# Kernel optimization log

Hardware: AMD Instinct MI355X
Metric: run time of the kernel (lower is better)

## Reference

```python
import jax, jax.numpy as jnp
import numpy as np


def _conv1x1(x, w):
    # x [N,I,D,H,W], w [O,I]
    return jnp.einsum('nidhw,oi->nodhw', x, w)


def _conv3x3(x, w):
    return jax.lax.conv_general_dilated(
        x, w, window_strides=(1, 1, 1), padding=[(1, 1)] * 3,
        dimension_numbers=('NCDHW', 'OIDHW', 'NCDHW'))


def _interp_axis(x, out_len, axis):
    # linear interpolation along one axis, align_corners=True
    in_len = x.shape[axis]
    scale = (in_len - 1) / (out_len - 1)
    pos = jnp.arange(out_len, dtype=x.dtype) * scale
    lo = jnp.clip(jnp.floor(pos).astype(jnp.int32), 0, in_len - 1)
    hi = jnp.minimum(lo + 1, in_len - 1)
    frac = pos - lo.astype(x.dtype)
    shp = [1] * x.ndim
    shp[axis] = out_len
    frac = frac.reshape(shp)
    return jnp.take(x, lo, axis=axis) * (1 - frac) + jnp.take(x, hi, axis=axis) * frac


def _upsample_trilinear_ac(x, size):
    for ax, s in zip((2, 3, 4), size):
        x = _interp_axis(x, s, ax)
    return x


def _grid_sample_3d(inp, grid):
    # inp [N,C,D,H,W]; grid [N,Do,Ho,Wo,3] with channels (x=w, y=h, z=d) in [-1,1]
    # matches torch grid_sample defaults: trilinear, align_corners=False, zeros padding
    N, C, D, H, W = inp.shape
    ix = ((grid[..., 0] + 1) * W - 1) * 0.5
    iy = ((grid[..., 1] + 1) * H - 1) * 0.5
    iz = ((grid[..., 2] + 1) * D - 1) * 0.5
    x0 = jnp.floor(ix).astype(jnp.int32)
    y0 = jnp.floor(iy).astype(jnp.int32)
    z0 = jnp.floor(iz).astype(jnp.int32)
    fx = ix - x0.astype(inp.dtype)
    fy = iy - y0.astype(inp.dtype)
    fz = iz - z0.astype(inp.dtype)
    flat = inp.reshape(N, C, D * H * W)
    out = jnp.zeros((N, C) + grid.shape[1:4], dtype=inp.dtype)
    for dz, wz in ((0, 1 - fz), (1, fz)):
        for dy, wy in ((0, 1 - fy), (1, fy)):
            for dx, wx in ((0, 1 - fx), (1, fx)):
                zc = z0 + dz
                yc = y0 + dy
                xc = x0 + dx
                valid = (zc >= 0) & (zc < D) & (yc >= 0) & (yc < H) & (xc >= 0) & (xc < W)
                idx = (jnp.clip(zc, 0, D - 1) * H + jnp.clip(yc, 0, H - 1)) * W + jnp.clip(xc, 0, W - 1)
                vals = jax.vmap(lambda f, i: f[:, i])(flat, idx)  # [N,C,Do,Ho,Wo]
                w = (wz * wy * wx) * valid.astype(inp.dtype)
                out = out + vals * w[:, None]
    return out


def _point_reinforce(x, w_atten, w_conv):
    # SE-style: global avg pool -> 1x1 conv -> sigmoid -> residual scale -> 1x1 conv
    pooled = jnp.mean(x, axis=(2, 3, 4), keepdims=True)
    atten = jax.nn.sigmoid(_conv1x1(pooled, w_atten))
    x = x + x * atten
    return _conv1x1(x, w_conv)


def _forward(x, y, w_down_h, w_down_l, w_flow, w_att_atten, w_att_conv):
    D, H, W = x.shape[2:]
    low = _conv1x1(x, w_down_l)
    low = _point_reinforce(low, w_att_atten, w_att_conv)
    hf = _conv1x1(y, w_down_h)
    hf = _upsample_trilinear_ac(hf, (D, H, W))
    flow = _conv3x3(jnp.concatenate([hf, low], axis=1), w_flow)  # [N,3,D,H,W]
    # coordinate grid, channel order (w, h, d) as in the original flow_warp
    gw = jnp.broadcast_to(jnp.arange(W, dtype=x.dtype)[None, None, :], (D, H, W))
    gh = jnp.broadcast_to(jnp.arange(H, dtype=x.dtype)[None, :, None], (D, H, W))
    gd = jnp.broadcast_to(jnp.arange(D, dtype=x.dtype)[:, None, None], (D, H, W))
    grid = jnp.stack([gw, gh, gd], axis=0)[None]  # [1,3,D,H,W]
    norm = jnp.array([W, H, D], dtype=x.dtype)
    # NOTE: faithful to original -- divides by size only (grid ends up in [0,1), not [-1,1])
    vgrid = jnp.transpose(grid + flow, (0, 2, 3, 4, 1)) / norm  # [N,D,H,W,3]
    return _grid_sample_3d(y, vgrid)


def setup_inputs() -> dict:
    key = jax.random.key(0)
    ks = jax.random.split(key, 7)
    inplane_l, inplane_h, outplane = 64, 128, 64
    x = jax.random.normal(ks[0], (2, inplane_l, 16, 64, 64), dtype=jnp.float32)
    y = jax.random.normal(ks[1], (2, inplane_h, 8, 32, 32), dtype=jnp.float32)
    s = 0.05
    w_down_h = jax.random.normal(ks[2], (outplane, inplane_h), dtype=jnp.float32) * s
    w_down_l = jax.random.normal(ks[3], (outplane, inplane_l), dtype=jnp.float32) * s
    w_flow = jax.random.normal(ks[4], (3, 2 * outplane, 3, 3, 3), dtype=jnp.float32) * s
    w_att_atten = jax.random.normal(ks[5], (inplane_l, inplane_l), dtype=jnp.float32) * s
    w_att_conv = jax.random.normal(ks[6], (inplane_l, inplane_l), dtype=jnp.float32) * s
    return {'x': x, 'y': y, 'w_down_h': w_down_h, 'w_down_l': w_down_l,
            'w_flow': w_flow, 'w_att_atten': w_att_atten, 'w_att_conv': w_att_conv}


def reference(x, y, w_down_h, w_down_l, w_flow, w_att_atten, w_att_conv):
    return _forward(x, y, w_down_h, w_down_l, w_flow, w_att_atten, w_att_conv)
```

## Files before the change

### kernel.cpp

```cpp
#include <hip/hip_runtime.h>
#include <math.h>


#define MEANX_OFF  0
#define WCOMBT_OFF 128
#define HF_OFF     8320
#define LOW2_OFF   1056896
#define HFUP_OFF   9445504
#define VG_OFF     17834112
#define ZPAGE_OFF  18227328

__global__ void kmean(const float* __restrict__ x, float* __restrict__ meanx,
                      float* __restrict__ zpage) {
    if (blockIdx.x == 0 && threadIdx.x < 64) zpage[threadIdx.x] = 0.f;
    int ch = blockIdx.x;
    const float4* base = (const float4*)(x + (size_t)ch * 65536);
    float s = 0.f;
    for (int j = threadIdx.x; j < 16384; j += 256) {
        float4 v = base[j];
        s += v.x + v.y + v.z + v.w;
    }
    __shared__ float red[256];
    red[threadIdx.x] = s;
    __syncthreads();
    for (int off = 128; off > 0; off >>= 1) {
        if (threadIdx.x < off) red[threadIdx.x] += red[threadIdx.x + off];
        __syncthreads();
    }
    if (threadIdx.x == 0) meanx[ch] = red[0] * (1.0f / 65536.0f);
}

__global__ __launch_bounds__(256) void kprep(const float* __restrict__ wdl,
                                             const float* __restrict__ watt,
                                             const float* __restrict__ wconv,
                                             const float* __restrict__ meanx,
                                             float* __restrict__ wcombT) {
    const int n = blockIdx.x;
    const int tid = threadIdx.x;
    __shared__ float s_wdl[4096];
    __shared__ float s_wcT[4096];
    __shared__ float pooled[64], sc[64];
    for (int k = tid; k < 4096; k += 256) {
        s_wdl[k] = wdl[k];
        int o = k >> 6, j = k & 63;
        s_wcT[j * 64 + o] = wconv[k];
    }
    __syncthreads();
    if (tid < 64) {
        float p = 0.f;
        for (int i = 0; i < 64; ++i) p += s_wdl[tid * 64 + i] * meanx[n * 64 + i];
        pooled[tid] = p;
    }
    __syncthreads();
    if (tid < 64) {
        float a = 0.f;
        for (int i = 0; i < 64; ++i) a += watt[tid * 64 + i] * pooled[i];
        sc[tid] = 1.f + 1.f / (1.f + expf(-a));
    }
    __syncthreads();
    for (int k = 0; k < 16; ++k) {
        const int idx = tid + 256 * k;
        const int o = idx & 63, i = idx >> 6;
        float acc = 0.f;
#pragma unroll 8
        for (int j = 0; j < 64; ++j)
            acc += s_wcT[j * 64 + o] * (sc[j] * s_wdl[j * 64 + i]);
        wcombT[n * 4096 + i * 64 + o] = acc;
    }
}

__global__ __launch_bounds__(256) void kconv1l(const float* __restrict__ x,
                                               const float* __restrict__ wcombT,
                                               float* __restrict__ low2) {
    const int b = blockIdx.x;
    const int n = b >> 9;
    const int r = b & 511;
    const int os = r & 1;
    const int tile = r >> 1;
    const int p = tile * 256 + threadIdx.x;
    const float* xb = x + (size_t)n * 64 * 65536 + p;
    const float* wr = wcombT + n * 4096 + os * 32;

    float acc[32];
#pragma unroll
    for (int o = 0; o < 32; ++o) acc[o] = 0.f;

    for (int i = 0; i < 64; i += 2) {
        const float xi0 = xb[(size_t)(i + 0) * 65536];
        const float xi1 = xb[(size_t)(i + 1) * 65536];
#pragma unroll
        for (int o = 0; o < 32; ++o) {
            acc[o] = fmaf(wr[(i + 0) * 64 + o], xi0, acc[o]);
            acc[o] = fmaf(wr[(i + 1) * 64 + o], xi1, acc[o]);
        }
    }
    float* ob = low2 + (size_t)(n * 64 + os * 32) * 65536 + p;
#pragma unroll
    for (int o = 0; o < 32; ++o)
        ob[(size_t)o * 65536] = acc[o];
}

__global__ __launch_bounds__(256) void kconvh(const float* __restrict__ y,
                                              const float* __restrict__ wdh,
                                              float* __restrict__ hf) {
    const int b = blockIdx.x;
    const int n = b >> 7;
    const int r = b & 127;
    const int os = r & 3;
    const int tile = r >> 2;
    const int p = tile * 256 + threadIdx.x;
    const float* yb = y + (size_t)n * 128 * 8192 + p;

    float acc[16];
#pragma unroll
    for (int o = 0; o < 16; ++o) acc[o] = 0.f;

    for (int i = 0; i < 128; i += 2) {
        const float yi0 = yb[(size_t)(i + 0) * 8192];
        const float yi1 = yb[(size_t)(i + 1) * 8192];
#pragma unroll
        for (int o = 0; o < 16; ++o) {
            acc[o] = fmaf(wdh[(os * 16 + o) * 128 + i + 0], yi0, acc[o]);
            acc[o] = fmaf(wdh[(os * 16 + o) * 128 + i + 1], yi1, acc[o]);
        }
    }
    float* ob = hf + (size_t)(n * 64 + os * 16) * 8192 + p;
#pragma unroll
    for (int o = 0; o < 16; ++o)
        ob[(size_t)o * 8192] = acc[o];
}

__global__ __launch_bounds__(256) void kups(const float* __restrict__ hf,
                                            float* __restrict__ hfup) {
    int id2 = blockIdx.x * 256 + threadIdx.x;
    int wp = id2 & 31, h = (id2 >> 5) & 63, d = (id2 >> 11) & 15;
    int c = (id2 >> 15) & 63, n = id2 >> 21;
    const float SD = 7.0f / 15.0f, SH = 31.0f / 63.0f;
    float pd = (float)d * SD, ph = (float)h * SH;
    int z0 = (int)pd; if (z0 > 7) z0 = 7;
    int z1 = min(z0 + 1, 7); float fz = pd - (float)z0;
    int y0 = (int)ph; if (y0 > 31) y0 = 31;
    int y1 = min(y0 + 1, 31); float fy = ph - (float)y0;

    const int w0i = 2 * wp, w1i = 2 * wp + 1;
    float pw0 = (float)w0i * SH, pw1 = (float)w1i * SH;
    int xa = (int)pw0; if (xa > 31) xa = 31;
    float fx0 = pw0 - (float)xa;
    int xb = (int)pw1; if (xb > 31) xb = 31;
    float fx1 = pw1 - (float)xb;

    const float* b = hf + (size_t)(n * 64 + c) * 8192;
    const int r00 = (z0 * 32 + y0) * 32, r01 = (z0 * 32 + y1) * 32;
    const int r10 = (z1 * 32 + y0) * 32, r11 = (z1 * 32 + y1) * 32;
    const float wzy00 = (1.f - fz) * (1.f - fy), wzy01 = (1.f - fz) * fy;
    const float wzy10 = fz * (1.f - fy), wzy11 = fz * fy;

    float colv[3];
#pragma unroll
    for (int j = 0; j < 3; ++j) {
        int xc = min(xa + j, 31);
        colv[j] = wzy00 * b[r00 + xc] + wzy01 * b[r01 + xc] +
                  wzy10 * b[r10 + xc] + wzy11 * b[r11 + xc];
    }
    float o0 = colv[0] + (colv[1] - colv[0]) * fx0;
    int i1 = xb - xa;
    float lo = (i1 == 0) ? colv[0] : colv[1];
    float hi = (i1 == 0) ? colv[1] : colv[2];
    float o1 = lo + (hi - lo) * fx1;

    *(float2*)(hfup + ((size_t)id2 * 2)) = make_float2(o0, o1);
}

__global__ __launch_bounds__(256) void kflowp(const float* __restrict__ ws,
                                              const float* __restrict__ wflow,
                                              float* __restrict__ part) {
    const int tid = threadIdx.x;
    const int b = blockIdx.x;
    const int split = b & 15;
    const int tile = b >> 4;
    const int n = tile >> 6;
    const int t = tile & 63;
    const int td = t >> 4, th = (t >> 2) & 3, tw = t & 3;
    const int d0 = td * 4, h0 = th * 16, w0 = tw * 16;
    const int xo = tid & 3, ty = (tid >> 2) & 15, tz = tid >> 6;
    const int wv = tid >> 6;

    __shared__ float lds[3][2048];

    const int srcb = (split < 8)
        ? HFUP_OFF + (n * 64 + split * 8) * 65536
        : LOW2_OFF + (n * 64 + (split - 8) * 8) * 65536;

    int woff[8];
#pragma unroll
    for (int k = 0; k < 8; ++k) {
        const int e = tid + 256 * k;
        const int r = e / 18;
        const int lx = e - r * 18;
        const int z = r / 18;
        const int ly = r - z * 18;
        const int gz = d0 - 1 + z, gy = h0 - 1 + ly, gx = w0 - 1 + lx;
        const bool ok = (e < 1944) && ((unsigned)gz < 16u) && ((unsigned)gy < 64u) &&
                        ((unsigned)gx < 64u);
        woff[k] = ok ? (srcb + gz * 4096 + gy * 64 + gx) : ZPAGE_OFF;
    }

#define STAGE(BUFI, CI)                                                               \
    {                                                                                 \
        _Pragma("unroll")                                                             \
        for (int k = 0; k < 8; ++k) {                                                 \
            const int off = woff[k] + ((woff[k] < ZPAGE_OFF) ? (CI) * 65536 : 0);     \
            __builtin_amdgcn_global_load_lds(                                         \
                (const __attribute__((address_space(1))) unsigned int*)(ws + off),    \
                (__attribute__((address_space(3))) unsigned int*)                     \
                    (&lds[BUFI][wv * 64 + 256 * k]),                                  \
                4, 0, 0);                                                             \
        }                                                                             \
    }

    float acc[3][4];
#pragma unroll
    for (int o = 0; o < 3; ++o)
#pragma unroll
        for (int j = 0; j < 4; ++j) acc[o][j] = 0.f;

    STAGE(0, 0);

    for (int ci = 0; ci < 8; ++ci) {
        const int cur = ci % 3;
        if (ci < 7) {
            STAGE((ci + 1) % 3, ci + 1);
            asm volatile("s_waitcnt vmcnt(8)" ::: "memory");
        } else {
            asm volatile("s_waitcnt vmcnt(0)" ::: "memory");
        }
        __builtin_amdgcn_s_barrier();
        __builtin_amdgcn_sched_barrier(0);

        const int cgs = __builtin_amdgcn_readfirstlane(split * 8 + ci);
        const float* wb = wflow + (size_t)cgs * 27;
        const float* buf = lds[cur];
#pragma unroll
        for (int dz = 0; dz < 3; ++dz) {
#pragma unroll
            for (int dy = 0; dy < 3; ++dy) {
                const float* rp = &buf[((tz + dz) * 18 + ty + dy) * 18 + 4 * xo];
                const float2 a0 = *(const float2*)(rp);
                const float2 a1 = *(const float2*)(rp + 2);
                const float2 a2 = *(const float2*)(rp + 4);
                const float v[6] = {a0.x, a0.y, a1.x, a1.y, a2.x, a2.y};
                float wq[3][3];
#pragma unroll
                for (int o = 0; o < 3; ++o)
#pragma unroll
                    for (int dx = 0; dx < 3; ++dx)
                        wq[o][dx] = wb[o * 3456 + (dz * 3 + dy) * 3 + dx];
#pragma unroll
                for (int o = 0; o < 3; ++o)
#pragma unroll
                    for (int j = 0; j < 4; ++j)
#pragma unroll
                        for (int dx = 0; dx < 3; ++dx)
                            acc[o][j] = fmaf(wq[o][dx], v[j + dx], acc[o][j]);
            }
        }
    }
#undef STAGE

    const int oz = d0 + tz, oy = h0 + ty, ox = w0 + 4 * xo;
    const size_t base = ((size_t)(split * 2 + n)) * 3 * 65536;
    const int p = oz * 4096 + oy * 64 + ox;
#pragma unroll
    for (int o = 0; o < 3; ++o)
        *(float4*)(part + base + (size_t)o * 65536 + p) =
            make_float4(acc[o][0], acc[o][1], acc[o][2], acc[o][3]);
}

__global__ void kcomb(const float* __restrict__ part, float* __restrict__ vg) {
    int gid = blockIdx.x * 256 + threadIdx.x;
    int n = gid >> 16, p = gid & 65535;
    float s0 = 0.f, s1 = 0.f, s2 = 0.f;
    for (int s = 0; s < 16; ++s) {
        const float* bp = part + ((size_t)(s * 2 + n)) * 3 * 65536 + p;
        s0 += bp[0];
        s1 += bp[65536];
        s2 += bp[131072];
    }
    int w = p & 63, h = (p >> 6) & 63, d = p >> 12;
    size_t vb = (size_t)n * 3 * 65536;
    vg[vb + p]          = ((float)w + s0) * (1.0f / 64.0f);
    vg[vb + 65536 + p]  = ((float)h + s1) * (1.0f / 64.0f);
    vg[vb + 131072 + p] = ((float)d + s2) * (1.0f / 16.0f);
}

__global__ __launch_bounds__(256) void ktrans(const float* __restrict__ y,
                                              float* __restrict__ yt) {
    int b = blockIdx.x;
    int n = b >> 8;
    int rem = b & 255;
    int ct = rem >> 7, st = rem & 127;
    int c0 = ct * 64, s0 = st * 64;
    __shared__ float t[64][65];
    int tx = threadIdx.x & 63, ty = threadIdx.x >> 6;
#pragma unroll
    for (int k = 0; k < 16; ++k)
        t[ty + 4 * k][tx] = y[((size_t)(n * 128 + c0 + ty + 4 * k)) * 8192 + s0 + tx];
    __syncthreads();
#pragma unroll
    for (int k = 0; k < 16; ++k)
        yt[((size_t)(n * 8192 + s0 + ty + 4 * k)) * 128 + c0 + tx] = t[tx][ty + 4 * k];
}

__global__ __launch_bounds__(256) void ksample(const float* __restrict__ yt,
                                               const float* __restrict__ vg,
                                               float* __restrict__ out) {
    const int b = blockIdx.x;
    const int n = b >> 10;
    const int p0 = (b & 1023) << 6;
    const int tid = threadIdx.x;
    const int lane = tid & 63;
    const int wv = tid >> 6;

    __shared__ float lds[128 * 65];

    const float* ytn = yt + (size_t)n * 8192 * 128;
    const size_t vb = (size_t)n * 3 * 65536;

    for (int q = 0; q < 16; ++q) {
        const int pt = wv * 16 + q;
        const int p = p0 + pt;
        float gx = vg[vb + p], gy = vg[vb + 65536 + p], gz = vg[vb + 131072 + p];
        float ix = ((gx + 1.f) * 32.f - 1.f) * 0.5f;
        float iy = ((gy + 1.f) * 32.f - 1.f) * 0.5f;
        float iz = ((gz + 1.f) * 8.f - 1.f) * 0.5f;
        int x0 = (int)floorf(ix), y0 = (int)floorf(iy), z0 = (int)floorf(iz);
        float fx = ix - (float)x0, fy = iy - (float)y0, fz = iz - (float)z0;
        float wx[2] = {1.f - fx, fx}, wy[2] = {1.f - fy, fy}, wz[2] = {1.f - fz, fz};
        int idx8[8];
        float w8[8];
        float wsum = 0.f;
#pragma unroll
        for (int k = 0; k < 8; ++k) {
            int dz = k >> 2, dy = (k >> 1) & 1, dx = k & 1;
            int zc = z0 + dz, yc = y0 + dy, xc = x0 + dx;
            bool valid = ((unsigned)zc < 8u) && ((unsigned)yc < 32u) && ((unsigned)xc < 32u);
            int zcl = min(max(zc, 0), 7), ycl = min(max(yc, 0), 31), xcl = min(max(xc, 0), 31);
            idx8[k] = (zcl * 32 + ycl) * 32 + xcl;
            float wgt = wz[dz] * wy[dy] * wx[dx];
            w8[k] = valid ? wgt : 0.f;
            wsum += w8[k];
        }
        float ax = 0.f, ay = 0.f;
        if (wsum != 0.f) {
#pragma unroll
            for (int k = 0; k < 8; ++k) {
                const float2 v = *(const float2*)(ytn + (size_t)idx8[k] * 128 + 2 * lane);
                ax = fmaf(w8[k], v.x, ax);
                ay = fmaf(w8[k], v.y, ay);
            }
        }
        lds[(2 * lane) * 65 + pt] = ax;
        lds[(2 * lane + 1) * 65 + pt] = ay;
    }
    __syncthreads();
    const int pw = tid & 63, cw = tid >> 6;
    float* ob = out + (size_t)n * 128 * 65536 + p0 + pw;
#pragma unroll
    for (int k = 0; k < 32; ++k) {
        int c = k * 4 + cw;
        ob[(size_t)c * 65536] = lds[c * 65 + pw];
    }
}

extern "C" void kernel_launch(void* const* d_in, const int* in_sizes, int n_in,
                              void* d_out, int out_size, void* d_ws, size_t ws_size,
                              hipStream_t stream) {
    const float* x     = (const float*)d_in[0];
    const float* y     = (const float*)d_in[1];
    const float* wdh   = (const float*)d_in[2];
    const float* wdl   = (const float*)d_in[3];
    const float* wflow = (const float*)d_in[4];
    const float* watt  = (const float*)d_in[5];
    const float* wconv = (const float*)d_in[6];
    float* out = (float*)d_out;

    float* ws     = (float*)d_ws;
    float* meanx  = ws + MEANX_OFF;
    float* wcombT = ws + WCOMBT_OFF;
    float* hf     = ws + HF_OFF;
    float* low2   = ws + LOW2_OFF;
    float* hfup   = ws + HFUP_OFF;
    float* vg     = ws + VG_OFF;
    float* zpage  = ws + ZPAGE_OFF;

    float* part = out;
    float* yt = hfup;

    kmean<<<128, 256, 0, stream>>>(x, meanx, zpage);
    kprep<<<2, 256, 0, stream>>>(wdl, watt, wconv, meanx, wcombT);
    kconv1l<<<1024, 256, 0, stream>>>(x, wcombT, low2);
    kconvh<<<256, 256, 0, stream>>>(y, wdh, hf);
    kups<<<16384, 256, 0, stream>>>(hf, hfup);
    kflowp<<<2048, 256, 0, stream>>>(ws, wflow, part);
    kcomb<<<512, 256, 0, stream>>>(part, vg);
    ktrans<<<512, 256, 0, stream>>>(y, yt);
    ksample<<<2048, 256, 0, stream>>>(yt, vg, out);
}
```

Baseline: 195.8 us.

## Register-block two output depth slices per thread in flow conv, unroll 1x1 conv loops

```diff
diff --git a/kernel.cpp b/kernel.cpp
--- a/kernel.cpp
+++ b/kernel.cpp
@@ -85,13 +85,19 @@
 #pragma unroll
     for (int o = 0; o < 32; ++o) acc[o] = 0.f;
 
-    for (int i = 0; i < 64; i += 2) {
+    for (int i = 0; i < 64; i += 4) {
         const float xi0 = xb[(size_t)(i + 0) * 65536];
         const float xi1 = xb[(size_t)(i + 1) * 65536];
+        const float xi2 = xb[(size_t)(i + 2) * 65536];
+        const float xi3 = xb[(size_t)(i + 3) * 65536];
 #pragma unroll
         for (int o = 0; o < 32; ++o) {
-            acc[o] = fmaf(wr[(i + 0) * 64 + o], xi0, acc[o]);
-            acc[o] = fmaf(wr[(i + 1) * 64 + o], xi1, acc[o]);
+            float a = acc[o];
+            a = fmaf(wr[(i + 0) * 64 + o], xi0, a);
+            a = fmaf(wr[(i + 1) * 64 + o], xi1, a);
+            a = fmaf(wr[(i + 2) * 64 + o], xi2, a);
+            a = fmaf(wr[(i + 3) * 64 + o], xi3, a);
+            acc[o] = a;
         }
     }
     float* ob = low2 + (size_t)(n * 64 + os * 32) * 65536 + p;
@@ -115,13 +121,19 @@
 #pragma unroll
     for (int o = 0; o < 16; ++o) acc[o] = 0.f;
 
-    for (int i = 0; i < 128; i += 2) {
+    for (int i = 0; i < 128; i += 4) {
         const float yi0 = yb[(size_t)(i + 0) * 8192];
         const float yi1 = yb[(size_t)(i + 1) * 8192];
+        const float yi2 = yb[(size_t)(i + 2) * 8192];
+        const float yi3 = yb[(size_t)(i + 3) * 8192];
 #pragma unroll
         for (int o = 0; o < 16; ++o) {
-            acc[o] = fmaf(wdh[(os * 16 + o) * 128 + i + 0], yi0, acc[o]);
-            acc[o] = fmaf(wdh[(os * 16 + o) * 128 + i + 1], yi1, acc[o]);
+            float a = acc[o];
+            a = fmaf(wdh[(os * 16 + o) * 128 + i + 0], yi0, a);
+            a = fmaf(wdh[(os * 16 + o) * 128 + i + 1], yi1, a);
+            a = fmaf(wdh[(os * 16 + o) * 128 + i + 2], yi2, a);
+            a = fmaf(wdh[(os * 16 + o) * 128 + i + 3], yi3, a);
+            acc[o] = a;
         }
     }
     float* ob = hf + (size_t)(n * 64 + os * 16) * 8192 + p;
@@ -171,7 +183,7 @@
     *(float2*)(hfup + ((size_t)id2 * 2)) = make_float2(o0, o1);
 }
 
-__global__ __launch_bounds__(256) void kflowp(const float* __restrict__ ws,
+__global__ __launch_bounds__(128) void kflowp(const float* __restrict__ ws,
                                               const float* __restrict__ wflow,
                                               float* __restrict__ part) {
     const int tid = threadIdx.x;
@@ -182,7 +194,7 @@
     const int t = tile & 63;
     const int td = t >> 4, th = (t >> 2) & 3, tw = t & 3;
     const int d0 = td * 4, h0 = th * 16, w0 = tw * 16;
-    const int xo = tid & 3, ty = (tid >> 2) & 15, tz = tid >> 6;
+    const int xo = tid & 3, ty = (tid >> 2) & 15, tzp = tid >> 6;
     const int wv = tid >> 6;
 
     __shared__ float lds[3][2048];
@@ -191,10 +203,10 @@
         ? HFUP_OFF + (n * 64 + split * 8) * 65536
         : LOW2_OFF + (n * 64 + (split - 8) * 8) * 65536;
 
-    int woff[8];
-#pragma unroll
-    for (int k = 0; k < 8; ++k) {
-        const int e = tid + 256 * k;
+    int woff[16];
+#pragma unroll
+    for (int k = 0; k < 16; ++k) {
+        const int e = tid + 128 * k;
         const int r = e / 18;
         const int lx = e - r * 18;
         const int z = r / 18;
@@ -208,21 +220,23 @@
 #define STAGE(BUFI, CI)                                                               \
     {                                                                                 \
         _Pragma("unroll")                                                             \
-        for (int k = 0; k < 8; ++k) {                                                 \
+        for (int k = 0; k < 16; ++k) {                                                \
             const int off = woff[k] + ((woff[k] < ZPAGE_OFF) ? (CI) * 65536 : 0);     \
             __builtin_amdgcn_global_load_lds(                                         \
                 (const __attribute__((address_space(1))) unsigned int*)(ws + off),    \
                 (__attribute__((address_space(3))) unsigned int*)                     \
-                    (&lds[BUFI][wv * 64 + 256 * k]),                                  \
+                    (&lds[BUFI][wv * 64 + 128 * k]),                                  \
                 4, 0, 0);                                                             \
         }                                                                             \
     }
 
-    float acc[3][4];
+    float acc[3][2][4];
 #pragma unroll
     for (int o = 0; o < 3; ++o)
 #pragma unroll
-        for (int j = 0; j < 4; ++j) acc[o][j] = 0.f;
+        for (int q = 0; q < 2; ++q)
+#pragma unroll
+            for (int j = 0; j < 4; ++j) acc[o][q][j] = 0.f;
 
     STAGE(0, 0);
 
@@ -230,7 +244,7 @@
         const int cur = ci % 3;
         if (ci < 7) {
             STAGE((ci + 1) % 3, ci + 1);
-            asm volatile("s_waitcnt vmcnt(8)" ::: "memory");
+            asm volatile("s_waitcnt vmcnt(16)" ::: "memory");
         } else {
             asm volatile("s_waitcnt vmcnt(0)" ::: "memory");
         }
@@ -241,39 +255,49 @@
         const float* wb = wflow + (size_t)cgs * 27;
         const float* buf = lds[cur];
 #pragma unroll
-        for (int dz = 0; dz < 3; ++dz) {
+        for (int pi = 0; pi < 4; ++pi) {
+            const int pz = 2 * tzp + pi;
 #pragma unroll
             for (int dy = 0; dy < 3; ++dy) {
-                const float* rp = &buf[((tz + dz) * 18 + ty + dy) * 18 + 4 * xo];
+                const float* rp = &buf[(pz * 18 + ty + dy) * 18 + 4 * xo];
                 const float2 a0 = *(const float2*)(rp);
                 const float2 a1 = *(const float2*)(rp + 2);
                 const float2 a2 = *(const float2*)(rp + 4);
                 const float v[6] = {a0.x, a0.y, a1.x, a1.y, a2.x, a2.y};
-                float wq[3][3];
-#pragma unroll
-                for (int o = 0; o < 3; ++o)
-#pragma unroll
-                    for (int dx = 0; dx < 3; ++dx)
-                        wq[o][dx] = wb[o * 3456 + (dz * 3 + dy) * 3 + dx];
-#pragma unroll
-                for (int o = 0; o < 3; ++o)
-#pragma unroll
-                    for (int j = 0; j < 4; ++j)
-#pragma unroll
-                        for (int dx = 0; dx < 3; ++dx)
-                            acc[o][j] = fmaf(wq[o][dx], v[j + dx], acc[o][j]);
+#pragma unroll
+                for (int q = 0; q < 2; ++q) {
+                    const int dz = pi - q;
+                    if (dz < 0 || dz > 2) continue;
+#pragma unroll
+                    for (int o = 0; o < 3; ++o) {
+                        const float w0q = wb[o * 3456 + (dz * 3 + dy) * 3 + 0];
+                        const float w1q = wb[o * 3456 + (dz * 3 + dy) * 3 + 1];
+                        const float w2q = wb[o * 3456 + (dz * 3 + dy) * 3 + 2];
+#pragma unroll
+                        for (int j = 0; j < 4; ++j) {
+                            float a = acc[o][q][j];
+                            a = fmaf(w0q, v[j + 0], a);
+                            a = fmaf(w1q, v[j + 1], a);
+                            a = fmaf(w2q, v[j + 2], a);
+                            acc[o][q][j] = a;
+                        }
+                    }
+                }
             }
         }
     }
 #undef STAGE
 
-    const int oz = d0 + tz, oy = h0 + ty, ox = w0 + 4 * xo;
+    const int oy = h0 + ty, ox = w0 + 4 * xo;
     const size_t base = ((size_t)(split * 2 + n)) * 3 * 65536;
-    const int p = oz * 4096 + oy * 64 + ox;
 #pragma unroll
     for (int o = 0; o < 3; ++o)
-        *(float4*)(part + base + (size_t)o * 65536 + p) =
-            make_float4(acc[o][0], acc[o][1], acc[o][2], acc[o][3]);
+#pragma unroll
+        for (int q = 0; q < 2; ++q) {
+            const int oz = d0 + 2 * tzp + q;
+            *(float4*)(part + base + (size_t)o * 65536 + oz * 4096 + oy * 64 + ox) =
+                make_float4(acc[o][q][0], acc[o][q][1], acc[o][q][2], acc[o][q][3]);
+        }
 }
 
 __global__ void kcomb(const float* __restrict__ part, float* __restrict__ vg) {
@@ -401,7 +425,7 @@
     kconv1l<<<1024, 256, 0, stream>>>(x, wcombT, low2);
     kconvh<<<256, 256, 0, stream>>>(y, wdh, hf);
     kups<<<16384, 256, 0, stream>>>(hf, hfup);
-    kflowp<<<2048, 256, 0, stream>>>(ws, wflow, part);
+    kflowp<<<2048, 128, 0, stream>>>(ws, wflow, part);
     kcomb<<<512, 256, 0, stream>>>(part, vg);
     ktrans<<<512, 256, 0, stream>>>(y, yt);
     ksample<<<2048, 256, 0, stream>>>(yt, vg, out);
```

After: 208.5 us. +6.5%, slower.

## Merge independent kernels into combined launches via block-range dispatch

Applied to the files above, without the earlier changes.

```diff
diff --git a/kernel.cpp b/kernel.cpp
--- a/kernel.cpp
+++ b/kernel.cpp
@@ -10,24 +10,63 @@
 #define VG_OFF     17834112
 #define ZPAGE_OFF  18227328
 
-__global__ void kmean(const float* __restrict__ x, float* __restrict__ meanx,
-                      float* __restrict__ zpage) {
-    if (blockIdx.x == 0 && threadIdx.x < 64) zpage[threadIdx.x] = 0.f;
-    int ch = blockIdx.x;
-    const float4* base = (const float4*)(x + (size_t)ch * 65536);
-    float s = 0.f;
-    for (int j = threadIdx.x; j < 16384; j += 256) {
-        float4 v = base[j];
-        s += v.x + v.y + v.z + v.w;
-    }
-    __shared__ float red[256];
-    red[threadIdx.x] = s;
-    __syncthreads();
-    for (int off = 128; off > 0; off >>= 1) {
-        if (threadIdx.x < off) red[threadIdx.x] += red[threadIdx.x + off];
+__global__ __launch_bounds__(256) void kearly(const float* __restrict__ x,
+                                              const float* __restrict__ y,
+                                              const float* __restrict__ wdh,
+                                              float* __restrict__ meanx,
+                                              float* __restrict__ hf,
+                                              float* __restrict__ zpage) {
+    const int blk = blockIdx.x;
+    if (blk < 128) {
+        if (blk == 0 && threadIdx.x < 64) zpage[threadIdx.x] = 0.f;
+        int ch = blk;
+        const float4* base = (const float4*)(x + (size_t)ch * 65536);
+        float s = 0.f;
+        for (int j = threadIdx.x; j < 16384; j += 256) {
+            float4 v = base[j];
+            s += v.x + v.y + v.z + v.w;
+        }
+        __shared__ float red[256];
+        red[threadIdx.x] = s;
         __syncthreads();
-    }
-    if (threadIdx.x == 0) meanx[ch] = red[0] * (1.0f / 65536.0f);
+        for (int off = 128; off > 0; off >>= 1) {
+            if (threadIdx.x < off) red[threadIdx.x] += red[threadIdx.x + off];
+            __syncthreads();
+        }
+        if (threadIdx.x == 0) meanx[ch] = red[0] * (1.0f / 65536.0f);
+    } else {
+        const int b = blk - 128;
+        const int n = b >> 7;
+        const int r = b & 127;
+        const int os = r & 3;
+        const int tile = r >> 2;
+        const int p = tile * 256 + threadIdx.x;
+        const float* yb = y + (size_t)n * 128 * 8192 + p;
+
+        float acc[16];
+#pragma unroll
+        for (int o = 0; o < 16; ++o) acc[o] = 0.f;
+
+        for (int i = 0; i < 128; i += 4) {
+            const float yi0 = yb[(size_t)(i + 0) * 8192];
+            const float yi1 = yb[(size_t)(i + 1) * 8192];
+            const float yi2 = yb[(size_t)(i + 2) * 8192];
+            const float yi3 = yb[(size_t)(i + 3) * 8192];
+#pragma unroll
+            for (int o = 0; o < 16; ++o) {
+                float a = acc[o];
+                a = fmaf(wdh[(os * 16 + o) * 128 + i + 0], yi0, a);
+                a = fmaf(wdh[(os * 16 + o) * 128 + i + 1], yi1, a);
+                a = fmaf(wdh[(os * 16 + o) * 128 + i + 2], yi2, a);
+                a = fmaf(wdh[(os * 16 + o) * 128 + i + 3], yi3, a);
+                acc[o] = a;
+            }
+        }
+        float* ob = hf + (size_t)(n * 64 + os * 16) * 8192 + p;
+#pragma unroll
+        for (int o = 0; o < 16; ++o)
+            ob[(size_t)o * 8192] = acc[o];
+    }
 }
 
 __global__ __launch_bounds__(256) void kprep(const float* __restrict__ wdl,
@@ -69,106 +108,84 @@
     }
 }
 
-__global__ __launch_bounds__(256) void kconv1l(const float* __restrict__ x,
-                                               const float* __restrict__ wcombT,
-                                               float* __restrict__ low2) {
-    const int b = blockIdx.x;
-    const int n = b >> 9;
-    const int r = b & 511;
-    const int os = r & 1;
-    const int tile = r >> 1;
-    const int p = tile * 256 + threadIdx.x;
-    const float* xb = x + (size_t)n * 64 * 65536 + p;
-    const float* wr = wcombT + n * 4096 + os * 32;
-
-    float acc[32];
-#pragma unroll
-    for (int o = 0; o < 32; ++o) acc[o] = 0.f;
-
-    for (int i = 0; i < 64; i += 2) {
-        const float xi0 = xb[(size_t)(i + 0) * 65536];
-        const float xi1 = xb[(size_t)(i + 1) * 65536];
-#pragma unroll
-        for (int o = 0; o < 32; ++o) {
-            acc[o] = fmaf(wr[(i + 0) * 64 + o], xi0, acc[o]);
-            acc[o] = fmaf(wr[(i + 1) * 64 + o], xi1, acc[o]);
-        }
-    }
-    float* ob = low2 + (size_t)(n * 64 + os * 32) * 65536 + p;
-#pragma unroll
-    for (int o = 0; o < 32; ++o)
-        ob[(size_t)o * 65536] = acc[o];
-}
-
-__global__ __launch_bounds__(256) void kconvh(const float* __restrict__ y,
-                                              const float* __restrict__ wdh,
-                                              float* __restrict__ hf) {
-    const int b = blockIdx.x;
-    const int n = b >> 7;
-    const int r = b & 127;
-    const int os = r & 3;
-    const int tile = r >> 2;
-    const int p = tile * 256 + threadIdx.x;
-    const float* yb = y + (size_t)n * 128 * 8192 + p;
-
-    float acc[16];
-#pragma unroll
-    for (int o = 0; o < 16; ++o) acc[o] = 0.f;
-
-    for (int i = 0; i < 128; i += 2) {
-        const float yi0 = yb[(size_t)(i + 0) * 8192];
-        const float yi1 = yb[(size_t)(i + 1) * 8192];
-#pragma unroll
-        for (int o = 0; o < 16; ++o) {
-            acc[o] = fmaf(wdh[(os * 16 + o) * 128 + i + 0], yi0, acc[o]);
-            acc[o] = fmaf(wdh[(os * 16 + o) * 128 + i + 1], yi1, acc[o]);
-        }
-    }
-    float* ob = hf + (size_t)(n * 64 + os * 16) * 8192 + p;
-#pragma unroll
-    for (int o = 0; o < 16; ++o)
-        ob[(size_t)o * 8192] = acc[o];
-}
-
-__global__ __launch_bounds__(256) void kups(const float* __restrict__ hf,
+__global__ __launch_bounds__(256) void kmid(const float* __restrict__ x,
+                                            const float* __restrict__ wcombT,
+                                            const float* __restrict__ hf,
+                                            float* __restrict__ low2,
                                             float* __restrict__ hfup) {
-    int id2 = blockIdx.x * 256 + threadIdx.x;
-    int wp = id2 & 31, h = (id2 >> 5) & 63, d = (id2 >> 11) & 15;
-    int c = (id2 >> 15) & 63, n = id2 >> 21;
-    const float SD = 7.0f / 15.0f, SH = 31.0f / 63.0f;
-    float pd = (float)d * SD, ph = (float)h * SH;
-    int z0 = (int)pd; if (z0 > 7) z0 = 7;
-    int z1 = min(z0 + 1, 7); float fz = pd - (float)z0;
-    int y0 = (int)ph; if (y0 > 31) y0 = 31;
-    int y1 = min(y0 + 1, 31); float fy = ph - (float)y0;
-
-    const int w0i = 2 * wp, w1i = 2 * wp + 1;
-    float pw0 = (float)w0i * SH, pw1 = (float)w1i * SH;
-    int xa = (int)pw0; if (xa > 31) xa = 31;
-    float fx0 = pw0 - (float)xa;
-    int xb = (int)pw1; if (xb > 31) xb = 31;
-    float fx1 = pw1 - (float)xb;
-
-    const float* b = hf + (size_t)(n * 64 + c) * 8192;
-    const int r00 = (z0 * 32 + y0) * 32, r01 = (z0 * 32 + y1) * 32;
-    const int r10 = (z1 * 32 + y0) * 32, r11 = (z1 * 32 + y1) * 32;
-    const float wzy00 = (1.f - fz) * (1.f - fy), wzy01 = (1.f - fz) * fy;
-    const float wzy10 = fz * (1.f - fy), wzy11 = fz * fy;
-
-    float colv[3];
-#pragma unroll
-    for (int j = 0; j < 3; ++j) {
-        int xc = min(xa + j, 31);
-        colv[j] = wzy00 * b[r00 + xc] + wzy01 * b[r01 + xc] +
-                  wzy10 * b[r10 + xc] + wzy11 * b[r11 + xc];
-    }
-    float o0 = colv[0] + (colv[1] - colv[0]) * fx0;
-    int i1 = xb - xa;
-    float lo = (i1 == 0) ? colv[0] : colv[1];
-    float hi = (i1 == 0) ? colv[1] : colv[2];
-    float o1 = lo + (hi - lo) * fx1;
-
-    *(float2*)(hfup + ((size_t)id2 * 2)) = make_float2(o0, o1);
+    const int blk = blockIdx.x;
+    if (blk < 1024) {
+        const int b = blk;
+        const int n = b >> 9;
+        const int r = b & 511;
+        const int os = r & 1;
+        const int tile = r >> 1;
+        const int p = tile * 256 + threadIdx.x;
+        const float* xb = x + (size_t)n * 64 * 65536 + p;
+        const float* wr = wcombT + n * 4096 + os * 32;
+
+        float acc[32];
+#pragma unroll
+        for (int o = 0; o < 32; ++o) acc[o] = 0.f;
+
+        for (int i = 0; i < 64; i += 4) {
+            const float xi0 = xb[(size_t)(i + 0) * 65536];
+            const float xi1 = xb[(size_t)(i + 1) * 65536];
+            const float xi2 = xb[(size_t)(i + 2) * 65536];
+            const float xi3 = xb[(size_t)(i + 3) * 65536];
+#pragma unroll
+            for (int o = 0; o < 32; ++o) {
+                float a = acc[o];
+                a = fmaf(wr[(i + 0) * 64 + o], xi0, a);
+                a = fmaf(wr[(i + 1) * 64 + o], xi1, a);
+                a = fmaf(wr[(i + 2) * 64 + o], xi2, a);
+                a = fmaf(wr[(i + 3) * 64 + o], xi3, a);
+                acc[o] = a;
+            }
+        }
+        float* ob = low2 + (size_t)(n * 64 + os * 32) * 65536 + p;
+#pragma unroll
+        for (int o = 0; o < 32; ++o)
+            ob[(size_t)o * 65536] = acc[o];
+    } else {
+        int id2 = (blk - 1024) * 256 + threadIdx.x;
+        int wp = id2 & 31, h = (id2 >> 5) & 63, d = (id2 >> 11) & 15;
+        int c = (id2 >> 15) & 63, n = id2 >> 21;
+        const float SD = 7.0f / 15.0f, SH = 31.0f / 63.0f;
+        float pd = (float)d * SD, ph = (float)h * SH;
+        int z0 = (int)pd; if (z0 > 7) z0 = 7;
+        int z1 = min(z0 + 1, 7); float fz = pd - (float)z0;
+        int y0 = (int)ph; if (y0 > 31) y0 = 31;
+        int y1 = min(y0 + 1, 31); float fy = ph - (float)y0;
+
+        const int w0i = 2 * wp, w1i = 2 * wp + 1;
+        float pw0 = (float)w0i * SH, pw1 = (float)w1i * SH;
+        int xa = (int)pw0; if (xa > 31) xa = 31;
+        float fx0 = pw0 - (float)xa;
+        int xb2 = (int)pw1; if (xb2 > 31) xb2 = 31;
+        float fx1 = pw1 - (float)xb2;
+
+        const float* b = hf + (size_t)(n * 64 + c) * 8192;
+        const int r00 = (z0 * 32 + y0) * 32, r01 = (z0 * 32 + y1) * 32;
+        const int r10 = (z1 * 32 + y0) * 32, r11 = (z1 * 32 + y1) * 32;
+        const float wzy00 = (1.f - fz) * (1.f - fy), wzy01 = (1.f - fz) * fy;
+        const float wzy10 = fz * (1.f - fy), wzy11 = fz * fy;
+
+        float colv[3];
+#pragma unroll
+        for (int j = 0; j < 3; ++j) {
+            int xc = min(xa + j, 31);
+            colv[j] = wzy00 * b[r00 + xc] + wzy01 * b[r01 + xc] +
+                      wzy10 * b[r10 + xc] + wzy11 * b[r11 + xc];
+        }
+        float o0 = colv[0] + (colv[1] - colv[0]) * fx0;
+        int i1 = xb2 - xa;
+        float lo = (i1 == 0) ? colv[0] : colv[1];
+        float hi = (i1 == 0) ? colv[1] : colv[2];
+        float o1 = lo + (hi - lo) * fx1;
+
+        *(float2*)(hfup + ((size_t)id2 * 2)) = make_float2(o0, o1);
+    }
 }
 
 __global__ __launch_bounds__(256) void kflowp(const float* __restrict__ ws,
@@ -276,39 +293,42 @@
             make_float4(acc[o][0], acc[o][1], acc[o][2], acc[o][3]);
 }
 
-__global__ void kcomb(const float* __restrict__ part, float* __restrict__ vg) {
-    int gid = blockIdx.x * 256 + threadIdx.x;
-    int n = gid >> 16, p = gid & 65535;
-    float s0 = 0.f, s1 = 0.f, s2 = 0.f;
-    for (int s = 0; s < 16; ++s) {
-        const float* bp = part + ((size_t)(s * 2 + n)) * 3 * 65536 + p;
-        s0 += bp[0];
-        s1 += bp[65536];
-        s2 += bp[131072];
-    }
-    int w = p & 63, h = (p >> 6) & 63, d = p >> 12;
-    size_t vb = (size_t)n * 3 * 65536;
-    vg[vb + p]          = ((float)w + s0) * (1.0f / 64.0f);
-    vg[vb + 65536 + p]  = ((float)h + s1) * (1.0f / 64.0f);
-    vg[vb + 131072 + p] = ((float)d + s2) * (1.0f / 16.0f);
-}
-
-__global__ __launch_bounds__(256) void ktrans(const float* __restrict__ y,
-                                              float* __restrict__ yt) {
-    int b = blockIdx.x;
-    int n = b >> 8;
-    int rem = b & 255;
-    int ct = rem >> 7, st = rem & 127;
-    int c0 = ct * 64, s0 = st * 64;
-    __shared__ float t[64][65];
-    int tx = threadIdx.x & 63, ty = threadIdx.x >> 6;
-#pragma unroll
-    for (int k = 0; k < 16; ++k)
-        t[ty + 4 * k][tx] = y[((size_t)(n * 128 + c0 + ty + 4 * k)) * 8192 + s0 + tx];
-    __syncthreads();
-#pragma unroll
-    for (int k = 0; k < 16; ++k)
-        yt[((size_t)(n * 8192 + s0 + ty + 4 * k)) * 128 + c0 + tx] = t[tx][ty + 4 * k];
+__global__ __launch_bounds__(256) void kpost(const float* __restrict__ part,
+                                             const float* __restrict__ y,
+                                             float* __restrict__ vg,
+                                             float* __restrict__ yt) {
+    const int blk = blockIdx.x;
+    if (blk < 512) {
+        int gid = blk * 256 + threadIdx.x;
+        int n = gid >> 16, p = gid & 65535;
+        float s0 = 0.f, s1 = 0.f, s2 = 0.f;
+        for (int s = 0; s < 16; ++s) {
+            const float* bp = part + ((size_t)(s * 2 + n)) * 3 * 65536 + p;
+            s0 += bp[0];
+            s1 += bp[65536];
+            s2 += bp[131072];
+        }
+        int w = p & 63, h = (p >> 6) & 63, d = p >> 12;
+        size_t vb = (size_t)n * 3 * 65536;
+        vg[vb + p]          = ((float)w + s0) * (1.0f / 64.0f);
+        vg[vb + 65536 + p]  = ((float)h + s1) * (1.0f / 64.0f);
+        vg[vb + 131072 + p] = ((float)d + s2) * (1.0f / 16.0f);
+    } else {
+        int b = blk - 512;
+        int n = b >> 8;
+        int rem = b & 255;
+        int ct = rem >> 7, st = rem & 127;
+        int c0 = ct * 64, s0 = st * 64;
+        __shared__ float t[64][65];
+        int tx = threadIdx.x & 63, ty = threadIdx.x >> 6;
+#pragma unroll
+        for (int k = 0; k < 16; ++k)
+            t[ty + 4 * k][tx] = y[((size_t)(n * 128 + c0 + ty + 4 * k)) * 8192 + s0 + tx];
+        __syncthreads();
+#pragma unroll
+        for (int k = 0; k < 16; ++k)
+            yt[((size_t)(n * 8192 + s0 + ty + 4 * k)) * 128 + c0 + tx] = t[tx][ty + 4 * k];
+    }
 }
 
 __global__ __launch_bounds__(256) void ksample(const float* __restrict__ yt,
@@ -396,13 +416,10 @@
     float* part = out;
     float* yt = hfup;
 
-    kmean<<<128, 256, 0, stream>>>(x, meanx, zpage);
+    kearly<<<384, 256, 0, stream>>>(x, y, wdh, meanx, hf, zpage);
     kprep<<<2, 256, 0, stream>>>(wdl, watt, wconv, meanx, wcombT);
-    kconv1l<<<1024, 256, 0, stream>>>(x, wcombT, low2);
-    kconvh<<<256, 256, 0, stream>>>(y, wdh, hf);
-    kups<<<16384, 256, 0, stream>>>(hf, hfup);
+    kmid<<<17408, 256, 0, stream>>>(x, wcombT, hf, low2, hfup);
     kflowp<<<2048, 256, 0, stream>>>(ws, wflow, part);
-    kcomb<<<512, 256, 0, stream>>>(part, vg);
-    ktrans<<<512, 256, 0, stream>>>(y, yt);
+    kpost<<<1024, 256, 0, stream>>>(part, y, vg, yt);
     ksample<<<2048, 256, 0, stream>>>(yt, vg, out);
 }
```

After: 172.9 us. -11.7%, faster.
